# Optimization experiments

Hardware: AMD Instinct MI355X
Metric: run time of the kernel (lower is better)

The kernel has to match this reference:

```python
import jax, jax.numpy as jnp
import numpy as np

ALPHA = 0.25
GAMMA = 2.0
EPS = 1e-8


def _lsa(cost):
    """Jonker-Volgenant shortest-augmenting-path linear sum assignment.
    Matches scipy.optimize.linear_sum_assignment for rectangular matrices."""
    cost = np.asarray(cost, dtype=np.float64)
    transposed = cost.shape[0] > cost.shape[1]
    if transposed:
        cost = cost.T
    n, m = cost.shape  # n <= m
    INF = 1e18
    u = np.zeros(n + 1)
    v = np.zeros(m + 1)
    p = np.zeros(m + 1, dtype=np.int64)   # p[j] = row (1-indexed) assigned to col j
    way = np.zeros(m + 1, dtype=np.int64)
    for i in range(1, n + 1):
        p[0] = i
        j0 = 0
        minv = np.full(m + 1, INF)
        used = np.zeros(m + 1, dtype=bool)
        while True:
            used[j0] = True
            i0 = p[j0]
            cur = cost[i0 - 1] - u[i0] - v[1:]
            free = ~used[1:]
            better = free & (cur < minv[1:])
            minv[1:][better] = cur[better]
            way[1:][better] = j0
            masked = np.where(free, minv[1:], INF)
            j1 = int(np.argmin(masked)) + 1
            delta = masked[j1 - 1]
            u[p[used]] += delta
            v[used] -= delta
            minv[1:][free] -= delta
            j0 = j1
            if p[j0] == 0:
                break
        while j0 != 0:  # augment
            j1 = way[j0]
            p[j0] = p[j1]
            j0 = j1
    row_of_col = p[1:] - 1
    cols = np.nonzero(row_of_col >= 0)[0]
    rows = row_of_col[cols]
    if transposed:
        rows, cols = cols, rows
    order = np.argsort(rows)
    return rows[order], cols[order]


def _focal_cost(p):
    """pos_cost - neg_cost for sigmoid probs p, per focal-loss matcher cost."""
    neg = (1.0 - ALPHA) * p ** GAMMA * (-jnp.log(1.0 - p + EPS))
    pos = ALPHA * (1.0 - p) ** GAMMA * (-jnp.log(p + EPS))
    return pos - neg


def _match(rec, loc, targets):
    """rec: [bs, Q, Crec] logits; loc: [bs, Q, Cloc] logits; targets: [bs, nt] int.
    Returns (src_idx, tgt_idx) each [bs, nt] (query index, target index)."""
    nt = targets.shape[1]
    cost_class = jnp.take_along_axis(_focal_cost(jax.nn.sigmoid(rec)),
                                     targets[:, None, :], axis=2)      # [bs, Q, nt]
    cost_pos = _focal_cost(jax.nn.sigmoid(loc))[:, :, :nt]             # tgt_pos = arange(nt)
    C = np.asarray(2.0 * cost_class + cost_pos)                        # [bs, Q, nt]
    src, tgt = [], []
    for b in range(C.shape[0]):  # per-batch Hungarian, as in original
        r, c = _lsa(C[b])
        src.append(r)
        tgt.append(c)
    return jnp.asarray(np.stack(src)), jnp.asarray(np.stack(tgt))


def _ce(logits, labels):
    # F.cross_entropy with mean reduction
    logp = jax.nn.log_softmax(logits, axis=-1)
    return -jnp.mean(jnp.take_along_axis(logp, labels[..., None], axis=-1))


def setup_inputs() -> dict:
    key = jax.random.key(0)
    k1, k2, k3 = jax.random.split(key, 3)
    rec = jax.random.normal(k1, (128, 107, 32, 32), dtype=jnp.float32)
    loc = jax.random.normal(k2, (128, 25, 32, 32), dtype=jnp.float32)
    targets = jax.random.randint(k3, (128, 25), 0, 107, dtype=jnp.int64)
    return {"rec": rec, "loc": loc, "targets": targets}


def reference(rec, loc, targets):
    bs, c_rec, H, W = rec.shape
    c_loc = loc.shape[1]
    nt = targets.shape[1]
    rec = jnp.transpose(rec.reshape(bs, c_rec, H * W), (0, 2, 1))  # [bs, Q, Crec]
    loc = jnp.transpose(loc.reshape(bs, c_loc, H * W), (0, 2, 1))  # [bs, Q, Cloc]
    src_idx, tgt_idx = _match(rec, loc, targets)                   # [bs, nt] each
    rec_m = jnp.take_along_axis(rec, src_idx[:, :, None], axis=1)  # [bs, nt, Crec]
    loc_m = jnp.take_along_axis(loc, src_idx[:, :, None], axis=1)  # [bs, nt, Cloc]
    cls_labels = jnp.take_along_axis(targets, tgt_idx, axis=1)     # [bs, nt]
    pos_labels = tgt_idx                                           # tgt_pos[b, j] == j
    det_rec_losses = _ce(rec_m.reshape(bs * nt, c_rec), cls_labels.reshape(-1))
    pos_losses = _ce(loc_m.reshape(bs * nt, c_loc), pos_labels.reshape(-1))
    return (det_rec_losses, pos_losses)
```

## Files before the change

kernel.cpp:

```cpp
#include <hip/hip_runtime.h>
#include <hip/hip_bf16.h>
#include <math.h>

#define BS   128
#define NT   25
#define CREC 107
#define CLOC 25
#define QN   1024
#define INFD 1e18
#define WSTR 257
__device__ __forceinline__ int widx(int j) {
    int q = j - 1;
    return (q & 3) * WSTR + (q >> 2);
}

__device__ __forceinline__ float focal_cost_f(float x) {
    float p   = 1.0f / (1.0f + __expf(-x));
    float neg = 0.75f * p * p * (-__logf(1.0f - p + 1e-8f));
    float pos = 0.25f * (1.0f - p) * (1.0f - p) * (-__logf(p + 1e-8f));
    return pos - neg;
}

__global__ __launch_bounds__(256)
void rowmin_kernel(const float* __restrict__ rec, const float* __restrict__ loc,
                   const int* __restrict__ targets, float* __restrict__ cost_g,
                   float* __restrict__ rowmin_g, int* __restrict__ rowarg_g) {
    const int pid   = blockIdx.x;
    const int b     = pid / NT, r = pid % NT;
    const int tid   = threadIdx.x;
    const int qbase = tid << 2;
    const int tc    = targets[pid];

    float4 r4 = *(const float4*)(rec + ((size_t)b * CREC + tc) * QN + qbase);
    float4 l4 = *(const float4*)(loc + ((size_t)b * CLOC + r)  * QN + qbase);
    float4 c;
    c.x = 2.0f * focal_cost_f(r4.x) + focal_cost_f(l4.x);
    c.y = 2.0f * focal_cost_f(r4.y) + focal_cost_f(l4.y);
    c.z = 2.0f * focal_cost_f(r4.z) + focal_cost_f(l4.z);
    c.w = 2.0f * focal_cost_f(r4.w) + focal_cost_f(l4.w);
    *(float4*)(cost_g + ((size_t)pid << 10) + qbase) = c;

    float bv = c.x; int bq = qbase;
    if (c.y < bv) { bv = c.y; bq = qbase + 1; }
    if (c.z < bv) { bv = c.z; bq = qbase + 2; }
    if (c.w < bv) { bv = c.w; bq = qbase + 3; }
    #pragma unroll
    for (int off = 32; off; off >>= 1) {
        float ov = __shfl_xor(bv, off);
        int   oq = __shfl_xor(bq, off);
        if (ov < bv || (ov == bv && oq < bq)) { bv = ov; bq = oq; }
    }
    __shared__ float bmv[4];
    __shared__ int   bmq[4];
    if ((tid & 63) == 0) { bmv[tid >> 6] = bv; bmq[tid >> 6] = bq; }
    __syncthreads();
    if (tid == 0) {
        float fv = bmv[0]; int fq = bmq[0];
        #pragma unroll
        for (int w = 1; w < 4; ++w) {
            float ov = bmv[w]; int oq = bmq[w];
            if (ov < fv || (ov == fv && oq < fq)) { fv = ov; fq = oq; }
        }
        rowmin_g[pid] = fv; rowarg_g[pid] = fq;
    }
}

__global__ __launch_bounds__(256)
void search_kernel(const float* __restrict__ cost_g,
                   const float* __restrict__ rowmin_g, const int* __restrict__ rowarg_g,
                   int* __restrict__ pairq_g) {
    const int b     = blockIdx.x;
    const int tid   = threadIdx.x;
    const int wave  = tid >> 6;
    const int lane  = tid & 63;
    const int qbase = tid << 2;

    __shared__ int    way_s[4 * WSTR];
    __shared__ int    p_s[QN + 1];
    __shared__ double u_s[NT + 1];
    __shared__ float  rowmin_s[NT];
    __shared__ int    rowarg_s[NT];
    __shared__ int    unassigned_s[NT];
    __shared__ int    nun_s;
    __shared__ double candv_s[2][4];
    __shared__ int    candj_s[2][4];

    for (int j = tid; j <= QN; j += 256) p_s[j] = 0;
    if (tid < NT) {
        rowmin_s[tid] = rowmin_g[b * NT + tid];
        rowarg_s[tid] = rowarg_g[b * NT + tid];
    }
    __syncthreads();

    if (tid == 0) {
        nun_s = 0;
        for (int r = 0; r < NT; ++r) {
            u_s[r + 1] = (double)rowmin_s[r];
            int j = rowarg_s[r] + 1;
            if (p_s[j] == 0) p_s[j] = r + 1;
            else             unassigned_s[nun_s++] = r + 1;
        }
    }
    __syncthreads();
    const int nun = nun_s;

    const float* cb = cost_g + ((size_t)b * NT << 10);

    double v[4] = {0.0, 0.0, 0.0, 0.0};

    for (int s = 0; s < nun; ++s) {
        const int i = unassigned_s[s];
        double minv[4] = {INFD, INFD, INFD, INFD};
        double snap[4] = {0.0, 0.0, 0.0, 0.0};
        double dsum    = 0.0;
        unsigned usedmask = 0;
        int j0 = 0;
        int parity = 0;

        for (;;) {
            int i0;
            if (j0 == 0) {
                i0 = i;
            } else {
                int q0 = j0 - 1;
                if ((q0 >> 2) == tid) {
                    int m = q0 & 3;
                    usedmask |= 1u << m;
                    minv[m] = INFD;
                    snap[m] = dsum;
                }
                i0 = p_s[j0];
            }
            const double ui0 = u_s[i0];
            const float4 c4 = *(const float4*)(cb + ((size_t)(i0 - 1) << 10) + qbase);
            const float cf[4] = { c4.x, c4.y, c4.z, c4.w };

            double bestv = INFD; int bestj = QN + 2;
            #pragma unroll
            for (int m = 0; m < 4; ++m) {
                if (!(usedmask & (1u << m))) {
                    const int j = qbase + m + 1;
                    double cur = (double)cf[m] - ui0 - v[m];
                    if (cur < minv[m]) { minv[m] = cur; way_s[widx(j)] = j0; }
                    double mv = minv[m];
                    if (mv < bestv || (mv == bestv && j < bestj)) { bestv = mv; bestj = j; }
                }
            }

            float own32 = (float)bestv;
            float w32 = own32;
            #pragma unroll
            for (int off = 32; off; off >>= 1) w32 = fminf(w32, __shfl_xor(w32, off));
            unsigned long long cand = __ballot(own32 == w32);
            double wv = INFD; int wj = QN + 2;
            while (cand) {
                int l = __ffsll(cand) - 1; cand &= cand - 1;
                double vv = __shfl(bestv, l);
                int    jj = __shfl(bestj, l);
                if (vv < wv || (vv == wv && jj < wj)) { wv = vv; wj = jj; }
            }
            if (lane == 0) { candv_s[parity][wave] = wv; candj_s[parity][wave] = wj; }
            __syncthreads();
            double delta = candv_s[parity][0]; int j1 = candj_s[parity][0];
            #pragma unroll
            for (int w = 1; w < 4; ++w) {
                double dv = candv_s[parity][w]; int dj = candj_s[parity][w];
                if (dv < delta || (dv == delta && dj < j1)) { delta = dv; j1 = dj; }
            }
            parity ^= 1;
            dsum += delta;

            #pragma unroll
            for (int m = 0; m < 4; ++m) {
                if (usedmask & (1u << m)) v[m]    -= delta;
                else                      minv[m] -= delta;
            }
            j0 = j1;
            if (p_s[j0] == 0) break;
        }

        if (tid == 0) u_s[i] += dsum;
        unsigned mm = usedmask;
        while (mm) {
            int m = __ffs(mm) - 1; mm &= mm - 1;
            u_s[p_s[qbase + m + 1]] += dsum - snap[m];
        }
        __syncthreads();
        if (tid == 0) {
            int jj = j0;
            while (jj != 0) {
                int jn = way_s[widx(jj)];
                p_s[jj] = (jn == 0) ? i : p_s[jn];
                jj = jn;
            }
        }
        __syncthreads();
    }

    for (int j = tid + 1; j <= QN; j += 256)
        if (p_s[j] > 0) pairq_g[b * NT + (p_s[j] - 1)] = j - 1;
}

__global__ __launch_bounds__(64)
void loss_kernel(const float* __restrict__ rec, const float* __restrict__ loc,
                 const int* __restrict__ targets, const int* __restrict__ pairq_g,
                 float* __restrict__ partial) {
    const int pid  = blockIdx.x;
    const int b    = pid / NT, t = pid % NT;
    const int lane = threadIdx.x;
    const int q    = pairq_g[pid];

    const float* rb = rec + (size_t)b * CREC * QN + q;
    float x0 = (lane < CREC)      ? rb[(size_t)lane * QN]        : -1e30f;
    float x1 = (lane + 64 < CREC) ? rb[(size_t)(lane + 64) * QN] : -1e30f;
    float mx = fmaxf(x0, x1);
    #pragma unroll
    for (int off = 32; off; off >>= 1) mx = fmaxf(mx, __shfl_xor(mx, off));
    float e = 0.0f;
    if (lane < CREC)      e += expf(x0 - mx);
    if (lane + 64 < CREC) e += expf(x1 - mx);
    #pragma unroll
    for (int off = 32; off; off >>= 1) e += __shfl_xor(e, off);
    float lse = mx + logf(e);

    const float* lb = loc + (size_t)b * CLOC * QN + q;
    float y = (lane < CLOC) ? lb[(size_t)lane * QN] : -1e30f;
    float my = y;
    #pragma unroll
    for (int off = 32; off; off >>= 1) my = fmaxf(my, __shfl_xor(my, off));
    float ey = (lane < CLOC) ? expf(y - my) : 0.0f;
    #pragma unroll
    for (int off = 32; off; off >>= 1) ey += __shfl_xor(ey, off);
    float lsey = my + logf(ey);

    if (lane == 0) {
        int lab = targets[pid];
        partial[pid]           = lse  - rb[(size_t)lab * QN];
        partial[BS * NT + pid] = lsey - lb[(size_t)t * QN];
    }
}

__global__ __launch_bounds__(256)
void finalize_kernel(const float* __restrict__ partial, float* __restrict__ out) {
    const int tid = threadIdx.x;
    float s0 = 0.0f, s1 = 0.0f;
    for (int i = tid; i < BS * NT; i += 256) {
        s0 += partial[i];
        s1 += partial[BS * NT + i];
    }
    __shared__ float a0[4], a1[4];
    #pragma unroll
    for (int off = 32; off; off >>= 1) { s0 += __shfl_xor(s0, off); s1 += __shfl_xor(s1, off); }
    if ((tid & 63) == 0) { a0[tid >> 6] = s0; a1[tid >> 6] = s1; }
    __syncthreads();
    if (tid == 0) {
        out[0] = (a0[0] + a0[1] + a0[2] + a0[3]) * (1.0f / (BS * NT));
        out[1] = (a1[0] + a1[1] + a1[2] + a1[3]) * (1.0f / (BS * NT));
    }
}

extern "C" void kernel_launch(void* const* d_in, const int* in_sizes, int n_in,
                              void* d_out, int out_size, void* d_ws, size_t ws_size,
                              hipStream_t stream) {
    (void)in_sizes; (void)n_in; (void)out_size; (void)ws_size;
    const float* rec     = (const float*)d_in[0];
    const float* loc     = (const float*)d_in[1];
    const int*   targets = (const int*)d_in[2];
    float* out = (float*)d_out;

    float* cost_g   = (float*)d_ws;
    float* rowmin_g = cost_g + (size_t)BS * NT * QN;
    int*   rowarg_g = (int*)(rowmin_g + BS * NT);
    int*   pairq_g  = rowarg_g + BS * NT;
    float* partial  = (float*)(pairq_g + BS * NT);

    hipLaunchKernelGGL(rowmin_kernel, dim3(BS * NT), dim3(256), 0, stream,
                       rec, loc, targets, cost_g, rowmin_g, rowarg_g);
    hipLaunchKernelGGL(search_kernel, dim3(BS), dim3(256), 0, stream,
                       cost_g, rowmin_g, rowarg_g, pairq_g);
    hipLaunchKernelGGL(loss_kernel, dim3(BS * NT), dim3(64), 0, stream,
                       rec, loc, targets, pairq_g, partial);
    hipLaunchKernelGGL(finalize_kernel, dim3(1), dim3(256), 0, stream,
                       partial, out);
}
```

Baseline: 141.5 us.

## Stage per-batch cost tile in LDS for JV search; fuse finalize via atomics

The search kernel now copies each batch's 25x1024 float cost tile (100 KB) into dynamic shared memory once, so the serial augmenting-path loop reads cost rows from LDS instead of global memory on every step. Separately, the finalize kernel is removed: the loss kernel accumulates scaled per-pair losses directly into the output with atomicAdd after a memset. This cuts latency on the critical serial search loop and one kernel launch. The trade-offs are a large LDS footprint per block, which relies on the MI355X's enlarged LDS, an extra memset launch, and nondeterministic float summation order.

```diff
diff --git a/kernel.cpp b/kernel.cpp
--- a/kernel.cpp
+++ b/kernel.cpp
@@ -69,6 +69,7 @@
 void search_kernel(const float* __restrict__ cost_g,
                    const float* __restrict__ rowmin_g, const int* __restrict__ rowarg_g,
                    int* __restrict__ pairq_g) {
+    extern __shared__ float cost_s[];
     const int b     = blockIdx.x;
     const int tid   = threadIdx.x;
     const int wave  = tid >> 6;
@@ -85,6 +86,12 @@
     __shared__ double candv_s[2][4];
     __shared__ int    candj_s[2][4];
 
+    {
+        const float4* src = (const float4*)(cost_g + ((size_t)b * NT << 10));
+        float4*       dst = (float4*)cost_s;
+        #pragma unroll
+        for (int k = 0; k < 25; ++k) dst[tid + 256 * k] = src[tid + 256 * k];
+    }
     for (int j = tid; j <= QN; j += 256) p_s[j] = 0;
     if (tid < NT) {
         rowmin_s[tid] = rowmin_g[b * NT + tid];
@@ -103,8 +110,6 @@
     }
     __syncthreads();
     const int nun = nun_s;
-
-    const float* cb = cost_g + ((size_t)b * NT << 10);
 
     double v[4] = {0.0, 0.0, 0.0, 0.0};
 
@@ -132,7 +137,7 @@
                 i0 = p_s[j0];
             }
             const double ui0 = u_s[i0];
-            const float4 c4 = *(const float4*)(cb + ((size_t)(i0 - 1) << 10) + qbase);
+            const float4 c4 = *(const float4*)(cost_s + ((i0 - 1) << 10) + qbase);
             const float cf[4] = { c4.x, c4.y, c4.z, c4.w };
 
             double bestv = INFD; int bestj = QN + 2;
@@ -204,7 +209,7 @@
 __global__ __launch_bounds__(64)
 void loss_kernel(const float* __restrict__ rec, const float* __restrict__ loc,
                  const int* __restrict__ targets, const int* __restrict__ pairq_g,
-                 float* __restrict__ partial) {
+                 float* __restrict__ out) {
     const int pid  = blockIdx.x;
     const int b    = pid / NT, t = pid % NT;
     const int lane = threadIdx.x;
@@ -235,27 +240,8 @@
 
     if (lane == 0) {
         int lab = targets[pid];
-        partial[pid]           = lse  - rb[(size_t)lab * QN];
-        partial[BS * NT + pid] = lsey - lb[(size_t)t * QN];
-    }
-}
-
-__global__ __launch_bounds__(256)
-void finalize_kernel(const float* __restrict__ partial, float* __restrict__ out) {
-    const int tid = threadIdx.x;
-    float s0 = 0.0f, s1 = 0.0f;
-    for (int i = tid; i < BS * NT; i += 256) {
-        s0 += partial[i];
-        s1 += partial[BS * NT + i];
-    }
-    __shared__ float a0[4], a1[4];
-    #pragma unroll
-    for (int off = 32; off; off >>= 1) { s0 += __shfl_xor(s0, off); s1 += __shfl_xor(s1, off); }
-    if ((tid & 63) == 0) { a0[tid >> 6] = s0; a1[tid >> 6] = s1; }
-    __syncthreads();
-    if (tid == 0) {
-        out[0] = (a0[0] + a0[1] + a0[2] + a0[3]) * (1.0f / (BS * NT));
-        out[1] = (a1[0] + a1[1] + a1[2] + a1[3]) * (1.0f / (BS * NT));
+        atomicAdd(&out[0], (lse  - rb[(size_t)lab * QN]) * (1.0f / (BS * NT)));
+        atomicAdd(&out[1], (lsey - lb[(size_t)t * QN])   * (1.0f / (BS * NT)));
     }
 }
 
@@ -272,14 +258,17 @@
     float* rowmin_g = cost_g + (size_t)BS * NT * QN;
     int*   rowarg_g = (int*)(rowmin_g + BS * NT);
     int*   pairq_g  = rowarg_g + BS * NT;
-    float* partial  = (float*)(pairq_g + BS * NT);
+
+    hipMemsetAsync(d_out, 0, 2 * sizeof(float), stream);
+
+    const int tile_bytes = NT * QN * (int)sizeof(float);
+    (void)hipFuncSetAttribute((const void*)search_kernel,
+                              hipFuncAttributeMaxDynamicSharedMemorySize, tile_bytes);
 
     hipLaunchKernelGGL(rowmin_kernel, dim3(BS * NT), dim3(256), 0, stream,
                        rec, loc, targets, cost_g, rowmin_g, rowarg_g);
-    hipLaunchKernelGGL(search_kernel, dim3(BS), dim3(256), 0, stream,
+    hipLaunchKernelGGL(search_kernel, dim3(BS), dim3(256), tile_bytes, stream,
                        cost_g, rowmin_g, rowarg_g, pairq_g);
     hipLaunchKernelGGL(loss_kernel, dim3(BS * NT), dim3(64), 0, stream,
-                       rec, loc, targets, pairq_g, partial);
-    hipLaunchKernelGGL(finalize_kernel, dim3(1), dim3(256), 0, stream,
-                       partial, out);
-}
+                       rec, loc, targets, pairq_g, out);
+}
```

After: 221.2 us. 1.56x slower.
